# Performance work log

Hardware: AMD Instinct MI355X
Metric: run time of the kernel (lower is better)

Reference implementation:

```python
import jax, jax.numpy as jnp
import numpy as np

C_IN, C_HID, N_HEADS, N, B = 128, 32, 4, 384, 1
INF = 1e9


def setup_inputs() -> dict:
    key = jax.random.key(0)
    ks = jax.random.split(key, 8)
    s = 1.0 / np.sqrt(C_IN)
    return {
        "z": jax.random.normal(ks[0], (B, N, N, C_IN), dtype=jnp.float32),
        "mask": jnp.ones((B, N, N), dtype=jnp.float32),
        "ln_w": jnp.ones((C_IN,), dtype=jnp.float32),
        "ln_b": jnp.zeros((C_IN,), dtype=jnp.float32),
        "w_tri": jax.random.normal(ks[1], (C_IN, N_HEADS), dtype=jnp.float32) * s,
        "wq": jax.random.normal(ks[2], (C_IN, N_HEADS * C_HID), dtype=jnp.float32) * s,
        "wk": jax.random.normal(ks[3], (C_IN, N_HEADS * C_HID), dtype=jnp.float32) * s,
        "wv": jax.random.normal(ks[4], (C_IN, N_HEADS * C_HID), dtype=jnp.float32) * s,
        "wg": jax.random.normal(ks[5], (C_IN, N_HEADS * C_HID), dtype=jnp.float32) * s,
        "wo": jax.random.normal(ks[6], (N_HEADS * C_HID, C_IN), dtype=jnp.float32) * s,
    }


def _layer_norm(x, w, b, eps=1e-5):
    mu = jnp.mean(x, axis=-1, keepdims=True)
    var = jnp.var(x, axis=-1, keepdims=True)
    return (x - mu) * jax.lax.rsqrt(var + eps) * w + b


def reference(z, mask, ln_w, ln_b, w_tri, wq, wk, wv, wg, wo):
    # starting=True: attend over J (last pair axis); batch dims are (B, I)
    zn = _layer_norm(z, ln_w, ln_b)                       # [B,I,J,C]
    # biases
    mask_bias = (INF * (mask - 1.0))[:, :, None, None, :]  # [B,I,1,1,J]
    tri = jnp.einsum("bijc,ch->bhij", zn, w_tri)[:, None]  # [B,1,H,I,J]
    # projections -> [B,I,J,H,Ch]
    shp = zn.shape[:-1] + (N_HEADS, C_HID)
    q = (zn @ wq).reshape(shp) * (1.0 / np.sqrt(C_HID))
    k = (zn @ wk).reshape(shp)
    v = (zn @ wv).reshape(shp)
    scores = jnp.einsum("biqhc,bikhc->bihqk", q, k) + mask_bias + tri  # [B,I,H,J,J]
    a = jax.nn.softmax(scores, axis=-1)
    o = jnp.einsum("bihqk,bikhc->biqhc", a, v).reshape(zn.shape[:-1] + (N_HEADS * C_HID,))
    g = jax.nn.sigmoid(zn @ wg)                           # gated output (OpenFold-style)
    return (o * g) @ wo                                    # [B,I,J,C_in]
```

## Files before the change

### kernel.cpp

```cpp
#include <hip/hip_runtime.h>
#include <hip/hip_bf16.h>

#define NN 384
#define CIN 128
#define NH 4
#define CH 32
#define NPOS (NN * NN)
#define INFB 1e9f
#define QSCALE 0.17677669529663687f

typedef float f32x4 __attribute__((ext_vector_type(4)));
typedef short short8 __attribute__((ext_vector_type(8)));

__device__ __forceinline__ float bf2f(unsigned short u) {
    return __uint_as_float(((unsigned int)u) << 16);
}
__device__ __forceinline__ unsigned short f2bf(float f) {
    unsigned int u = __float_as_uint(f);
    u += 0x7fffu + ((u >> 16) & 1u);
    return (unsigned short)(u >> 16);
}
__device__ __forceinline__ unsigned int pack2bf(float a, float b) {
    return (unsigned int)f2bf(a) | ((unsigned int)f2bf(b) << 16);
}

__global__ __launch_bounds__(256) void ln_kernel(
    const float* __restrict__ z, const float* __restrict__ lnw, const float* __restrict__ lnb,
    const float* __restrict__ wtri,
    unsigned short* __restrict__ zn, unsigned short* __restrict__ trib)
{
    __shared__ float zt[32 * CIN];
    __shared__ float mu_s[32], rs_s[32];
    __shared__ float wt_s[CIN * NH];
    const int t = threadIdx.x;
    const long base = (long)blockIdx.x * (32 * CIN);

    #pragma unroll
    for (int r = 0; r < 16; ++r) zt[t + 256 * r] = z[base + t + 256 * r];
    wt_s[t] = wtri[t]; wt_s[t + 256] = wtri[t + 256];
    __syncthreads();

    {
        int p = t >> 3, s = t & 7;
        float sum = 0.f, sq = 0.f;
        for (int c = s; c < CIN; c += 8) { float x = zt[p * CIN + c]; sum += x; sq += x * x; }
        #pragma unroll
        for (int m = 1; m < 8; m <<= 1) { sum += __shfl_xor(sum, m); sq += __shfl_xor(sq, m); }
        if (s == 0) {
            float mu = sum * (1.f / CIN);
            float var = sq * (1.f / CIN) - mu * mu;
            mu_s[p] = mu; rs_s[p] = rsqrtf(var + 1e-5f);
        }
    }
    __syncthreads();
    #pragma unroll
    for (int r = 0; r < 16; ++r) {
        int idx = t + 256 * r; int p = idx >> 7, c = idx & 127;
        zt[idx] = (zt[idx] - mu_s[p]) * rs_s[p] * lnw[c] + lnb[c];
    }
    __syncthreads();

    unsigned int* zno = (unsigned int*)zn + (long)blockIdx.x * 2048;
    #pragma unroll
    for (int r = 0; r < 8; ++r) {
        int i32 = t + 256 * r;
        zno[i32] = pack2bf(zt[2 * i32], zt[2 * i32 + 1]);
    }

    if (t < 128) {
        int h = t >> 5, p = t & 31;
        float acc = 0.f;
        #pragma unroll 8
        for (int ii = 0; ii < CIN; ++ii) {
            int ci = (p + ii) & 127;
            acc = fmaf(zt[p * CIN + ci], wt_s[ci * NH + h], acc);
        }
        trib[(long)h * NPOS + (long)blockIdx.x * 32 + p] = f2bf(acc);
    }
}

__global__ __launch_bounds__(256) void wconv_kernel(
    const float* __restrict__ wq, const float* __restrict__ wk, const float* __restrict__ wv,
    const float* __restrict__ wg, const float* __restrict__ wo,
    unsigned short* __restrict__ wcat, unsigned short* __restrict__ wot)
{
    const int m = blockIdx.x, t = threadIdx.x;
    const float* W = (m == 0) ? wq : (m == 1) ? wk : (m == 2) ? wv : (m == 3) ? wg : wo;
    const float s = (m == 0) ? QSCALE : 1.0f;
    unsigned short* dst = (m < 4) ? (wcat + m * CIN * CIN) : wot;
    for (int idx = t; idx < CIN * CIN; idx += 256) {
        int n = idx >> 7, k = idx & 127;
        dst[idx] = f2bf(W[k * CIN + n] * s);
    }
}

__device__ __forceinline__ void gemm128_core(
    const unsigned short* __restrict__ Ag, const unsigned short* __restrict__ Bg,
    unsigned short* lsA, unsigned short* lsB, f32x4 acc[4][4], int t)
{
    const int lane = t & 63, w = t >> 6, l15 = lane & 15, hi = lane >> 4;
    #pragma unroll
    for (int it = 0; it < 8; ++it) {
        int row = w * 32 + it * 4 + hi;
        int cb = l15 * 16;
        uint4 va = *(const uint4*)((const char*)Ag + row * 256 + cb);
        uint4 vb = *(const uint4*)((const char*)Bg + row * 256 + cb);
        int sw = cb ^ ((row & 7) << 4);
        *(uint4*)((char*)lsA + row * 256 + sw) = va;
        *(uint4*)((char*)lsB + row * 256 + sw) = vb;
    }
    __syncthreads();
    const int wm = (w >> 1) * 64, wn = (w & 1) * 64;
    #pragma unroll
    for (int kk = 0; kk < 4; ++kk) {
        short8 a[4], b[4];
        #pragma unroll
        for (int f = 0; f < 4; ++f) {
            int ra = wm + f * 16 + l15;
            int rb = wn + f * 16 + l15;
            int c = kk * 64 + hi * 16;
            a[f] = *(const short8*)((const char*)lsA + ra * 256 + (c ^ ((ra & 7) << 4)));
            b[f] = *(const short8*)((const char*)lsB + rb * 256 + (c ^ ((rb & 7) << 4)));
        }
        #pragma unroll
        for (int mf = 0; mf < 4; ++mf)
            #pragma unroll
            for (int nf = 0; nf < 4; ++nf)
                acc[mf][nf] = __builtin_amdgcn_mfma_f32_16x16x32_bf16(a[mf], b[nf], acc[mf][nf], 0, 0, 0);
    }
}

__global__ __launch_bounds__(256) void proj_gemm_kernel(
    const unsigned short* __restrict__ zn, const unsigned short* __restrict__ wcat,
    unsigned short* __restrict__ qb, unsigned short* __restrict__ kb,
    unsigned short* __restrict__ vb, unsigned short* __restrict__ gb)
{
    __shared__ alignas(16) unsigned short lsA[128 * 128];
    __shared__ alignas(16) unsigned short lsB[128 * 128];
    const int t = threadIdx.x;
    const int mb = blockIdx.x, mat = blockIdx.y;
    f32x4 acc[4][4];
    #pragma unroll
    for (int i = 0; i < 4; ++i)
        #pragma unroll
        for (int j = 0; j < 4; ++j) acc[i][j] = (f32x4){0.f, 0.f, 0.f, 0.f};
    gemm128_core(zn + (long)mb * 128 * 128, wcat + mat * 128 * 128, lsA, lsB, acc, t);

    const int lane = t & 63, w = t >> 6, l15 = lane & 15, hi = lane >> 4;
    const int wm = (w >> 1) * 64, wn = (w & 1) * 64;
    unsigned short* dst = (mat == 0) ? qb : (mat == 1) ? kb : (mat == 2) ? vb : gb;
    #pragma unroll
    for (int mf = 0; mf < 4; ++mf)
        #pragma unroll
        for (int nf = 0; nf < 4; ++nf)
            #pragma unroll
            for (int r = 0; r < 4; ++r) {
                long pos = (long)mb * 128 + wm + mf * 16 + hi * 4 + r;
                int n = wn + nf * 16 + l15;
                float v = acc[mf][nf][r];
                if (mat == 3) v = 1.f / (1.f + __expf(-v));
                dst[pos * CIN + n] = f2bf(v);
            }
}

__global__ __launch_bounds__(256) void attn_kernel(
    const unsigned short* __restrict__ qb, const unsigned short* __restrict__ kb,
    const unsigned short* __restrict__ vb, const unsigned short* __restrict__ trib,
    const float* __restrict__ mask, unsigned short* __restrict__ ob)
{
    constexpr int KP = 40;
    constexpr int VP = 392;
    constexpr int PP = 392;
    __shared__ alignas(16) unsigned short Ks[NN * KP];
    __shared__ alignas(16) unsigned short VTs[CH * VP];
    __shared__ alignas(16) unsigned short Ps[4][16 * PP];
    __shared__ float biasS[NN];

    const int t = threadIdx.x;
    const int i = blockIdx.x >> 2, h = blockIdx.x & 3;
    const long rowbase = (long)i * NN;

    {
        const unsigned int* ksrc = (const unsigned int*)kb + rowbase * (CIN / 2) + h * (CH / 2);
        for (int idx = t; idx < NN * 16; idx += 256) {
            int row = idx >> 4, c2 = idx & 15;
            *(unsigned int*)&Ks[row * KP + c2 * 2] = ksrc[(long)row * 64 + c2];
        }
        for (int idx = t; idx < CH * NN; idx += 256) {
            int n = idx >> 5, c = idx & 31;
            VTs[c * VP + n] = vb[(rowbase + n) * CIN + h * CH + c];
        }
        for (int idx = t; idx < NN; idx += 256)
            biasS[idx] = INFB * (mask[rowbase + idx] - 1.f);
    }
    __syncthreads();

    const int lane = t & 63, w = t >> 6, l15 = lane & 15, hi = lane >> 4;
    unsigned short* Pw = Ps[w];
    const f32x4 zero4 = {0.f, 0.f, 0.f, 0.f};

    for (int mt = w; mt < NN / 16; mt += 4) {
        const int q0 = mt * 16;

        {
            const uint4* tsrc = (const uint4*)(trib + (long)h * NPOS + (long)q0 * NN);
            uint4* tdst = (uint4*)Pw;
            #pragma unroll
            for (int it = 0; it < 12; ++it)
                tdst[it * 64 + lane] = tsrc[it * 64 + lane];
        }

        const short8 aq = *(const short8*)(qb + (rowbase + q0 + l15) * CIN + h * CH + hi * 8);

        f32x4 acc[24];
        #pragma unroll
        for (int nf = 0; nf < 24; ++nf) {
            const short8 bk = *(const short8*)&Ks[(nf * 16 + l15) * KP + hi * 8];
            acc[nf] = __builtin_amdgcn_mfma_f32_16x16x32_bf16(aq, bk, zero4, 0, 0, 0);
        }

        float mx[4] = {-1e30f, -1e30f, -1e30f, -1e30f};
        #pragma unroll
        for (int nf = 0; nf < 24; ++nf)
            #pragma unroll
            for (int r = 0; r < 4; ++r) {
                float s = acc[nf][r] + biasS[nf * 16 + l15]
                        + bf2f(Pw[(4 * hi + r) * 384 + nf * 16 + l15]);
                acc[nf][r] = s;
                mx[r] = fmaxf(mx[r], s);
            }
        #pragma unroll
        for (int m2 = 1; m2 < 16; m2 <<= 1)
            #pragma unroll
            for (int r = 0; r < 4; ++r) mx[r] = fmaxf(mx[r], __shfl_xor(mx[r], m2));

        float sum[4] = {0.f, 0.f, 0.f, 0.f};
        #pragma unroll
        for (int nf = 0; nf < 24; ++nf)
            #pragma unroll
            for (int r = 0; r < 4; ++r) {
                float e = __expf(acc[nf][r] - mx[r]);
                acc[nf][r] = e; sum[r] += e;
            }
        #pragma unroll
        for (int m2 = 1; m2 < 16; m2 <<= 1)
            #pragma unroll
            for (int r = 0; r < 4; ++r) sum[r] += __shfl_xor(sum[r], m2);
        float inv[4];
        #pragma unroll
        for (int r = 0; r < 4; ++r) inv[r] = 1.f / sum[r];

        #pragma unroll
        for (int nf = 0; nf < 24; ++nf)
            #pragma unroll
            for (int r = 0; r < 4; ++r)
                Pw[(4 * hi + r) * PP + nf * 16 + l15] = f2bf(acc[nf][r]);

        f32x4 o0 = zero4, o1 = zero4;
        #pragma unroll
        for (int ks = 0; ks < 12; ++ks) {
            const short8 ap  = *(const short8*)&Pw[l15 * PP + ks * 32 + hi * 8];
            const short8 bv0 = *(const short8*)&VTs[l15 * VP + ks * 32 + hi * 8];
            const short8 bv1 = *(const short8*)&VTs[(16 + l15) * VP + ks * 32 + hi * 8];
            o0 = __builtin_amdgcn_mfma_f32_16x16x32_bf16(ap, bv0, o0, 0, 0, 0);
            o1 = __builtin_amdgcn_mfma_f32_16x16x32_bf16(ap, bv1, o1, 0, 0, 0);
        }

        #pragma unroll
        for (int r = 0; r < 4; ++r) {
            long qrow = rowbase + q0 + 4 * hi + r;
            ob[qrow * CIN + h * CH + l15]      = f2bf(o0[r] * inv[r]);
            ob[qrow * CIN + h * CH + 16 + l15] = f2bf(o1[r] * inv[r]);
        }
    }
}

__global__ __launch_bounds__(256) void og_kernel(
    const unsigned int* __restrict__ ob, const unsigned int* __restrict__ gb,
    unsigned int* __restrict__ og)
{
    const int n32 = NPOS * CIN / 2;
    for (long idx = (long)blockIdx.x * 256 + threadIdx.x; idx < n32; idx += (long)gridDim.x * 256) {
        unsigned int o = ob[idx], g = gb[idx];
        og[idx] = pack2bf(bf2f((unsigned short)o) * bf2f((unsigned short)g),
                          bf2f((unsigned short)(o >> 16)) * bf2f((unsigned short)(g >> 16)));
    }
}

__global__ __launch_bounds__(256) void out_gemm_kernel(
    const unsigned short* __restrict__ og, const unsigned short* __restrict__ wot,
    float* __restrict__ out)
{
    __shared__ alignas(16) unsigned short lsA[128 * 128];
    __shared__ alignas(16) unsigned short lsB[128 * 128];
    const int t = threadIdx.x;
    const int mb = blockIdx.x;
    f32x4 acc[4][4];
    #pragma unroll
    for (int i = 0; i < 4; ++i)
        #pragma unroll
        for (int j = 0; j < 4; ++j) acc[i][j] = (f32x4){0.f, 0.f, 0.f, 0.f};
    gemm128_core(og + (long)mb * 128 * 128, wot, lsA, lsB, acc, t);

    const int lane = t & 63, w = t >> 6, l15 = lane & 15, hi = lane >> 4;
    const int wm = (w >> 1) * 64, wn = (w & 1) * 64;
    #pragma unroll
    for (int mf = 0; mf < 4; ++mf)
        #pragma unroll
        for (int nf = 0; nf < 4; ++nf)
            #pragma unroll
            for (int r = 0; r < 4; ++r) {
                long pos = (long)mb * 128 + wm + mf * 16 + hi * 4 + r;
                int n = wn + nf * 16 + l15;
                out[pos * CIN + n] = acc[mf][nf][r];
            }
}

extern "C" void kernel_launch(void* const* d_in, const int* in_sizes, int n_in,
                              void* d_out, int out_size, void* d_ws, size_t ws_size,
                              hipStream_t stream)
{
    const float* z    = (const float*)d_in[0];
    const float* mask = (const float*)d_in[1];
    const float* lnw  = (const float*)d_in[2];
    const float* lnb  = (const float*)d_in[3];
    const float* wtri = (const float*)d_in[4];
    const float* wq   = (const float*)d_in[5];
    const float* wk   = (const float*)d_in[6];
    const float* wv   = (const float*)d_in[7];
    const float* wg   = (const float*)d_in[8];
    const float* wo   = (const float*)d_in[9];
    float* out = (float*)d_out;

    char* ws = (char*)d_ws;
    size_t off = 0;
    auto carve = [&](size_t bytes) -> void* {
        void* p = ws + off; off += (bytes + 255) & ~size_t(255); return p;
    };
    const size_t nelem = (size_t)NPOS * CIN;
    unsigned short* zn  = (unsigned short*)carve(nelem * 2);
    unsigned short* qb  = (unsigned short*)carve(nelem * 2);
    unsigned short* kb  = (unsigned short*)carve(nelem * 2);
    unsigned short* vb  = (unsigned short*)carve(nelem * 2);
    unsigned short* gb  = (unsigned short*)carve(nelem * 2);
    unsigned short* ob  = (unsigned short*)carve(nelem * 2);
    unsigned short* trib = (unsigned short*)carve((size_t)NH * NPOS * 2);
    unsigned short* wcat = (unsigned short*)carve((size_t)4 * CIN * CIN * 2);
    unsigned short* wot  = (unsigned short*)carve((size_t)CIN * CIN * 2);
    (void)ws_size; (void)in_sizes; (void)n_in; (void)out_size;

    hipLaunchKernelGGL(ln_kernel, dim3(NPOS / 32), dim3(256), 0, stream,
                       z, lnw, lnb, wtri, zn, trib);
    hipLaunchKernelGGL(wconv_kernel, dim3(5), dim3(256), 0, stream,
                       wq, wk, wv, wg, wo, wcat, wot);
    hipLaunchKernelGGL(proj_gemm_kernel, dim3(NPOS / 128, 4), dim3(256), 0, stream,
                       zn, wcat, qb, kb, vb, gb);
    hipLaunchKernelGGL(attn_kernel, dim3(NN * NH), dim3(256), 0, stream,
                       qb, kb, vb, trib, mask, ob);
    hipLaunchKernelGGL(og_kernel, dim3(2048), dim3(256), 0, stream,
                       (const unsigned int*)ob, (const unsigned int*)gb, (unsigned int*)zn);
    hipLaunchKernelGGL(out_gemm_kernel, dim3(NPOS / 128), dim3(256), 0, stream,
                       (const unsigned short*)zn, wot, out);
}
```

Baseline: 460.8 us.

## Restructure pipeline: fuse gating into attention, tri-bias into projection GEMM, exp2 softmax

```diff
diff --git a/kernel.cpp b/kernel.cpp
--- a/kernel.cpp
+++ b/kernel.cpp
@@ -7,10 +7,13 @@
 #define CH 32
 #define NPOS (NN * NN)
 #define INFB 1e9f
+#define LOG2E 1.4426950408889634f
 #define QSCALE 0.17677669529663687f
+#define QSB (QSCALE * LOG2E)
 
 typedef float f32x4 __attribute__((ext_vector_type(4)));
-typedef short short8 __attribute__((ext_vector_type(8)));
+typedef short bf16x8 __attribute__((ext_vector_type(8)));
+typedef short bf16x4 __attribute__((ext_vector_type(4)));
 
 __device__ __forceinline__ float bf2f(unsigned short u) {
     return __uint_as_float(((unsigned int)u) << 16);
@@ -26,291 +29,320 @@
 
 __global__ __launch_bounds__(256) void ln_kernel(
     const float* __restrict__ z, const float* __restrict__ lnw, const float* __restrict__ lnb,
-    const float* __restrict__ wtri,
-    unsigned short* __restrict__ zn, unsigned short* __restrict__ trib)
-{
-    __shared__ float zt[32 * CIN];
-    __shared__ float mu_s[32], rs_s[32];
-    __shared__ float wt_s[CIN * NH];
+    unsigned short* __restrict__ zn)
+{
     const int t = threadIdx.x;
-    const long base = (long)blockIdx.x * (32 * CIN);
-
-    #pragma unroll
-    for (int r = 0; r < 16; ++r) zt[t + 256 * r] = z[base + t + 256 * r];
-    wt_s[t] = wtri[t]; wt_s[t + 256] = wtri[t + 256];
-    __syncthreads();
-
-    {
-        int p = t >> 3, s = t & 7;
-        float sum = 0.f, sq = 0.f;
-        for (int c = s; c < CIN; c += 8) { float x = zt[p * CIN + c]; sum += x; sq += x * x; }
-        #pragma unroll
-        for (int m = 1; m < 8; m <<= 1) { sum += __shfl_xor(sum, m); sq += __shfl_xor(sq, m); }
-        if (s == 0) {
-            float mu = sum * (1.f / CIN);
-            float var = sq * (1.f / CIN) - mu * mu;
-            mu_s[p] = mu; rs_s[p] = rsqrtf(var + 1e-5f);
-        }
-    }
-    __syncthreads();
-    #pragma unroll
-    for (int r = 0; r < 16; ++r) {
-        int idx = t + 256 * r; int p = idx >> 7, c = idx & 127;
-        zt[idx] = (zt[idx] - mu_s[p]) * rs_s[p] * lnw[c] + lnb[c];
-    }
-    __syncthreads();
-
-    unsigned int* zno = (unsigned int*)zn + (long)blockIdx.x * 2048;
-    #pragma unroll
-    for (int r = 0; r < 8; ++r) {
-        int i32 = t + 256 * r;
-        zno[i32] = pack2bf(zt[2 * i32], zt[2 * i32 + 1]);
-    }
-
-    if (t < 128) {
-        int h = t >> 5, p = t & 31;
-        float acc = 0.f;
-        #pragma unroll 8
-        for (int ii = 0; ii < CIN; ++ii) {
-            int ci = (p + ii) & 127;
-            acc = fmaf(zt[p * CIN + ci], wt_s[ci * NH + h], acc);
-        }
-        trib[(long)h * NPOS + (long)blockIdx.x * 32 + p] = f2bf(acc);
-    }
+    const int l31 = t & 31;
+    const f32x4 lw = *(const f32x4*)(lnw + l31 * 4);
+    const f32x4 lb = *(const f32x4*)(lnb + l31 * 4);
+    #pragma unroll
+    for (int it = 0; it < 4; ++it) {
+        long row = (long)blockIdx.x * 32 + it * 8 + (threadIdx.x >> 5);
+        f32x4 v = *(const f32x4*)(z + row * CIN + l31 * 4);
+        float s = v[0] + v[1] + v[2] + v[3];
+        float q = v[0]*v[0] + v[1]*v[1] + v[2]*v[2] + v[3]*v[3];
+        #pragma unroll
+        for (int m2 = 1; m2 < 32; m2 <<= 1) { s += __shfl_xor(s, m2); q += __shfl_xor(q, m2); }
+        float mu = s * (1.f / CIN);
+        float rs = rsqrtf(q * (1.f / CIN) - mu * mu + 1e-5f);
+        uint2 o;
+        o.x = pack2bf((v[0]-mu)*rs*lw[0]+lb[0], (v[1]-mu)*rs*lw[1]+lb[1]);
+        o.y = pack2bf((v[2]-mu)*rs*lw[2]+lb[2], (v[3]-mu)*rs*lw[3]+lb[3]);
+        *(uint2*)(zn + row * CIN + l31 * 4) = o;
+    }
+    (void)t;
 }
 
 __global__ __launch_bounds__(256) void wconv_kernel(
     const float* __restrict__ wq, const float* __restrict__ wk, const float* __restrict__ wv,
-    const float* __restrict__ wg, const float* __restrict__ wo,
+    const float* __restrict__ wg, const float* __restrict__ wtri, const float* __restrict__ wo,
     unsigned short* __restrict__ wcat, unsigned short* __restrict__ wot)
 {
     const int m = blockIdx.x, t = threadIdx.x;
-    const float* W = (m == 0) ? wq : (m == 1) ? wk : (m == 2) ? wv : (m == 3) ? wg : wo;
-    const float s = (m == 0) ? QSCALE : 1.0f;
-    unsigned short* dst = (m < 4) ? (wcat + m * CIN * CIN) : wot;
     for (int idx = t; idx < CIN * CIN; idx += 256) {
         int n = idx >> 7, k = idx & 127;
-        dst[idx] = f2bf(W[k * CIN + n] * s);
-    }
-}
-
-__device__ __forceinline__ void gemm128_core(
-    const unsigned short* __restrict__ Ag, const unsigned short* __restrict__ Bg,
-    unsigned short* lsA, unsigned short* lsB, f32x4 acc[4][4], int t)
-{
-    const int lane = t & 63, w = t >> 6, l15 = lane & 15, hi = lane >> 4;
-    #pragma unroll
-    for (int it = 0; it < 8; ++it) {
-        int row = w * 32 + it * 4 + hi;
-        int cb = l15 * 16;
-        uint4 va = *(const uint4*)((const char*)Ag + row * 256 + cb);
-        uint4 vb = *(const uint4*)((const char*)Bg + row * 256 + cb);
-        int sw = cb ^ ((row & 7) << 4);
-        *(uint4*)((char*)lsA + row * 256 + sw) = va;
-        *(uint4*)((char*)lsB + row * 256 + sw) = vb;
-    }
-    __syncthreads();
-    const int wm = (w >> 1) * 64, wn = (w & 1) * 64;
-    #pragma unroll
-    for (int kk = 0; kk < 4; ++kk) {
-        short8 a[4], b[4];
-        #pragma unroll
-        for (int f = 0; f < 4; ++f) {
-            int ra = wm + f * 16 + l15;
-            int rb = wn + f * 16 + l15;
-            int c = kk * 64 + hi * 16;
-            a[f] = *(const short8*)((const char*)lsA + ra * 256 + (c ^ ((ra & 7) << 4)));
-            b[f] = *(const short8*)((const char*)lsB + rb * 256 + (c ^ ((rb & 7) << 4)));
-        }
-        #pragma unroll
-        for (int mf = 0; mf < 4; ++mf)
-            #pragma unroll
-            for (int nf = 0; nf < 4; ++nf)
-                acc[mf][nf] = __builtin_amdgcn_mfma_f32_16x16x32_bf16(a[mf], b[nf], acc[mf][nf], 0, 0, 0);
-    }
-}
-
-__global__ __launch_bounds__(256) void proj_gemm_kernel(
+        if (m < 4) {
+            const float* W = (m == 0) ? wq : (m == 1) ? wk : (m == 2) ? wv : wg;
+            float s = (m == 0) ? QSB : 1.0f;
+            wcat[m * CIN * CIN + idx] = f2bf(W[k * CIN + n] * s);
+        } else if (m == 4) {
+            wcat[4 * CIN * CIN + idx] = (n < NH) ? f2bf(wtri[k * NH + n] * LOG2E) : (unsigned short)0;
+        } else {
+            wot[idx] = f2bf(wo[k * CIN + n]);
+        }
+    }
+}
+
+__global__ __launch_bounds__(256, 2) void proj_kernel(
     const unsigned short* __restrict__ zn, const unsigned short* __restrict__ wcat,
     unsigned short* __restrict__ qb, unsigned short* __restrict__ kb,
-    unsigned short* __restrict__ vb, unsigned short* __restrict__ gb)
-{
-    __shared__ alignas(16) unsigned short lsA[128 * 128];
-    __shared__ alignas(16) unsigned short lsB[128 * 128];
-    const int t = threadIdx.x;
-    const int mb = blockIdx.x, mat = blockIdx.y;
-    f32x4 acc[4][4];
-    #pragma unroll
-    for (int i = 0; i < 4; ++i)
-        #pragma unroll
-        for (int j = 0; j < 4; ++j) acc[i][j] = (f32x4){0.f, 0.f, 0.f, 0.f};
-    gemm128_core(zn + (long)mb * 128 * 128, wcat + mat * 128 * 128, lsA, lsB, acc, t);
-
-    const int lane = t & 63, w = t >> 6, l15 = lane & 15, hi = lane >> 4;
-    const int wm = (w >> 1) * 64, wn = (w & 1) * 64;
-    unsigned short* dst = (mat == 0) ? qb : (mat == 1) ? kb : (mat == 2) ? vb : gb;
-    #pragma unroll
-    for (int mf = 0; mf < 4; ++mf)
-        #pragma unroll
-        for (int nf = 0; nf < 4; ++nf)
-            #pragma unroll
-            for (int r = 0; r < 4; ++r) {
-                long pos = (long)mb * 128 + wm + mf * 16 + hi * 4 + r;
-                int n = wn + nf * 16 + l15;
-                float v = acc[mf][nf][r];
-                if (mat == 3) v = 1.f / (1.f + __expf(-v));
-                dst[pos * CIN + n] = f2bf(v);
-            }
-}
-
-__global__ __launch_bounds__(256) void attn_kernel(
-    const unsigned short* __restrict__ qb, const unsigned short* __restrict__ kb,
-    const unsigned short* __restrict__ vb, const unsigned short* __restrict__ trib,
-    const float* __restrict__ mask, unsigned short* __restrict__ ob)
-{
-    constexpr int KP = 40;
-    constexpr int VP = 392;
-    constexpr int PP = 392;
-    __shared__ alignas(16) unsigned short Ks[NN * KP];
-    __shared__ alignas(16) unsigned short VTs[CH * VP];
-    __shared__ alignas(16) unsigned short Ps[4][16 * PP];
-    __shared__ float biasS[NN];
-
-    const int t = threadIdx.x;
-    const int i = blockIdx.x >> 2, h = blockIdx.x & 3;
-    const long rowbase = (long)i * NN;
-
-    {
-        const unsigned int* ksrc = (const unsigned int*)kb + rowbase * (CIN / 2) + h * (CH / 2);
-        for (int idx = t; idx < NN * 16; idx += 256) {
-            int row = idx >> 4, c2 = idx & 15;
-            *(unsigned int*)&Ks[row * KP + c2 * 2] = ksrc[(long)row * 64 + c2];
-        }
-        for (int idx = t; idx < CH * NN; idx += 256) {
-            int n = idx >> 5, c = idx & 31;
-            VTs[c * VP + n] = vb[(rowbase + n) * CIN + h * CH + c];
-        }
-        for (int idx = t; idx < NN; idx += 256)
-            biasS[idx] = INFB * (mask[rowbase + idx] - 1.f);
-    }
-    __syncthreads();
-
-    const int lane = t & 63, w = t >> 6, l15 = lane & 15, hi = lane >> 4;
-    unsigned short* Pw = Ps[w];
-    const f32x4 zero4 = {0.f, 0.f, 0.f, 0.f};
-
-    for (int mt = w; mt < NN / 16; mt += 4) {
-        const int q0 = mt * 16;
-
-        {
-            const uint4* tsrc = (const uint4*)(trib + (long)h * NPOS + (long)q0 * NN);
-            uint4* tdst = (uint4*)Pw;
-            #pragma unroll
-            for (int it = 0; it < 12; ++it)
-                tdst[it * 64 + lane] = tsrc[it * 64 + lane];
-        }
-
-        const short8 aq = *(const short8*)(qb + (rowbase + q0 + l15) * CIN + h * CH + hi * 8);
-
-        f32x4 acc[24];
-        #pragma unroll
-        for (int nf = 0; nf < 24; ++nf) {
-            const short8 bk = *(const short8*)&Ks[(nf * 16 + l15) * KP + hi * 8];
-            acc[nf] = __builtin_amdgcn_mfma_f32_16x16x32_bf16(aq, bk, zero4, 0, 0, 0);
-        }
-
-        float mx[4] = {-1e30f, -1e30f, -1e30f, -1e30f};
-        #pragma unroll
-        for (int nf = 0; nf < 24; ++nf)
-            #pragma unroll
-            for (int r = 0; r < 4; ++r) {
-                float s = acc[nf][r] + biasS[nf * 16 + l15]
-                        + bf2f(Pw[(4 * hi + r) * 384 + nf * 16 + l15]);
-                acc[nf][r] = s;
-                mx[r] = fmaxf(mx[r], s);
-            }
-        #pragma unroll
-        for (int m2 = 1; m2 < 16; m2 <<= 1)
-            #pragma unroll
-            for (int r = 0; r < 4; ++r) mx[r] = fmaxf(mx[r], __shfl_xor(mx[r], m2));
-
-        float sum[4] = {0.f, 0.f, 0.f, 0.f};
-        #pragma unroll
-        for (int nf = 0; nf < 24; ++nf)
-            #pragma unroll
-            for (int r = 0; r < 4; ++r) {
-                float e = __expf(acc[nf][r] - mx[r]);
-                acc[nf][r] = e; sum[r] += e;
-            }
-        #pragma unroll
-        for (int m2 = 1; m2 < 16; m2 <<= 1)
-            #pragma unroll
-            for (int r = 0; r < 4; ++r) sum[r] += __shfl_xor(sum[r], m2);
-        float inv[4];
-        #pragma unroll
-        for (int r = 0; r < 4; ++r) inv[r] = 1.f / sum[r];
-
-        #pragma unroll
-        for (int nf = 0; nf < 24; ++nf)
-            #pragma unroll
-            for (int r = 0; r < 4; ++r)
-                Pw[(4 * hi + r) * PP + nf * 16 + l15] = f2bf(acc[nf][r]);
-
-        f32x4 o0 = zero4, o1 = zero4;
-        #pragma unroll
-        for (int ks = 0; ks < 12; ++ks) {
-            const short8 ap  = *(const short8*)&Pw[l15 * PP + ks * 32 + hi * 8];
-            const short8 bv0 = *(const short8*)&VTs[l15 * VP + ks * 32 + hi * 8];
-            const short8 bv1 = *(const short8*)&VTs[(16 + l15) * VP + ks * 32 + hi * 8];
-            o0 = __builtin_amdgcn_mfma_f32_16x16x32_bf16(ap, bv0, o0, 0, 0, 0);
-            o1 = __builtin_amdgcn_mfma_f32_16x16x32_bf16(ap, bv1, o1, 0, 0, 0);
-        }
-
-        #pragma unroll
-        for (int r = 0; r < 4; ++r) {
-            long qrow = rowbase + q0 + 4 * hi + r;
-            ob[qrow * CIN + h * CH + l15]      = f2bf(o0[r] * inv[r]);
-            ob[qrow * CIN + h * CH + 16 + l15] = f2bf(o1[r] * inv[r]);
-        }
-    }
-}
-
-__global__ __launch_bounds__(256) void og_kernel(
-    const unsigned int* __restrict__ ob, const unsigned int* __restrict__ gb,
-    unsigned int* __restrict__ og)
-{
-    const int n32 = NPOS * CIN / 2;
-    for (long idx = (long)blockIdx.x * 256 + threadIdx.x; idx < n32; idx += (long)gridDim.x * 256) {
-        unsigned int o = ob[idx], g = gb[idx];
-        og[idx] = pack2bf(bf2f((unsigned short)o) * bf2f((unsigned short)g),
-                          bf2f((unsigned short)(o >> 16)) * bf2f((unsigned short)(g >> 16)));
-    }
-}
-
-__global__ __launch_bounds__(256) void out_gemm_kernel(
-    const unsigned short* __restrict__ og, const unsigned short* __restrict__ wot,
-    float* __restrict__ out)
+    unsigned short* __restrict__ vb, unsigned short* __restrict__ gb,
+    unsigned short* __restrict__ trib)
 {
     __shared__ alignas(16) unsigned short lsA[128 * 128];
     __shared__ alignas(16) unsigned short lsB[128 * 128];
     const int t = threadIdx.x;
     const int mb = blockIdx.x;
+    const int lane = t & 63, w = t >> 6, l15 = lane & 15, hig = lane >> 4;
+
+    {
+        const unsigned short* Ag = zn + (long)mb * 16384;
+        #pragma unroll
+        for (int it = 0; it < 8; ++it) {
+            int row = w * 32 + it * 4 + hig; int cb = l15 * 16;
+            uint4 v = *(const uint4*)((const char*)Ag + row * 256 + cb);
+            *(uint4*)((char*)lsA + row * 256 + (cb ^ ((row & 7) << 4))) = v;
+        }
+    }
+    auto stageB = [&](int mat) {
+        const unsigned short* Bg = wcat + mat * 16384;
+        #pragma unroll
+        for (int it = 0; it < 8; ++it) {
+            int row = w * 32 + it * 4 + hig; int cb = l15 * 16;
+            uint4 v = *(const uint4*)((const char*)Bg + row * 256 + cb);
+            *(uint4*)((char*)lsB + row * 256 + (cb ^ ((row & 7) << 4))) = v;
+        }
+    };
+    stageB(0);
+    __syncthreads();
+
+    const int wm = (w >> 1) * 64, wn = (w & 1) * 64;
+    bf16x8 a[4][4];
+    #pragma unroll
+    for (int kk = 0; kk < 4; ++kk)
+        #pragma unroll
+        for (int mf = 0; mf < 4; ++mf) {
+            int ra = wm + mf * 16 + l15;
+            a[kk][mf] = *(const bf16x8*)((const char*)lsA + ra * 256 + ((kk * 64 + hig * 16) ^ ((ra & 7) << 4)));
+        }
+
+    for (int mat = 0;;) {
+        f32x4 acc[4][4];
+        #pragma unroll
+        for (int i = 0; i < 4; ++i)
+            #pragma unroll
+            for (int j = 0; j < 4; ++j) acc[i][j] = (f32x4){0.f, 0.f, 0.f, 0.f};
+        #pragma unroll
+        for (int kk = 0; kk < 4; ++kk) {
+            bf16x8 b[4];
+            #pragma unroll
+            for (int nf = 0; nf < 4; ++nf) {
+                int rb = wn + nf * 16 + l15;
+                b[nf] = *(const bf16x8*)((const char*)lsB + rb * 256 + ((kk * 64 + hig * 16) ^ ((rb & 7) << 4)));
+            }
+            #pragma unroll
+            for (int mf = 0; mf < 4; ++mf)
+                #pragma unroll
+                for (int nf = 0; nf < 4; ++nf)
+                    acc[mf][nf] = __builtin_amdgcn_mfma_f32_16x16x32_bf16(a[kk][mf], b[nf], acc[mf][nf], 0, 0, 0);
+        }
+        __syncthreads();
+        if (mat < 4) stageB(mat + 1);
+
+        if (mat < 4) {
+            unsigned short* dst = (mat == 0) ? qb : (mat == 1) ? kb : (mat == 2) ? vb : gb;
+            #pragma unroll
+            for (int mf = 0; mf < 4; ++mf)
+                #pragma unroll
+                for (int nf = 0; nf < 4; ++nf)
+                    #pragma unroll
+                    for (int r = 0; r < 4; ++r) {
+                        long pos = (long)mb * 128 + wm + mf * 16 + hig * 4 + r;
+                        int n = wn + nf * 16 + l15;
+                        float v = acc[mf][nf][r];
+                        if (mat == 3) v = 1.f / (1.f + __expf(-v));
+                        dst[pos * CIN + n] = f2bf(v);
+                    }
+        } else {
+            if (wn == 0 && l15 < NH) {
+                #pragma unroll
+                for (int mf = 0; mf < 4; ++mf)
+                    #pragma unroll
+                    for (int r = 0; r < 4; ++r) {
+                        long pos = (long)mb * 128 + wm + mf * 16 + hig * 4 + r;
+                        trib[(long)l15 * NPOS + pos] = f2bf(acc[mf][0][r]);
+                    }
+            }
+        }
+        if (mat == 4) break;
+        ++mat;
+        __syncthreads();
+    }
+}
+
+__global__ __launch_bounds__(256, 2) void attn_kernel(
+    const unsigned short* __restrict__ qb, const unsigned short* __restrict__ kb,
+    const unsigned short* __restrict__ vb, const unsigned short* __restrict__ gb,
+    const unsigned short* __restrict__ trib, const float* __restrict__ mask,
+    unsigned short* __restrict__ ogb)
+{
+    constexpr int KP = 40;
+    constexpr int VP = 392;
+    __shared__ alignas(16) unsigned short Ks[NN * KP];
+    __shared__ alignas(16) unsigned short VTs[CH * VP];
+    __shared__ alignas(16) unsigned short Ps[4][2][16 * 64];
+    __shared__ float biasS[NN];
+
+    const int t = threadIdx.x;
+    const int bid = blockIdx.x;
+    const int wg = (bid & 7) * 192 + (bid >> 3);
+    const int i = wg >> 2, h = wg & 3;
+    const long rowbase = (long)i * NN;
+
+    {
+        const unsigned int* ksrc = (const unsigned int*)kb + rowbase * 64 + h * 16;
+        for (int idx = t; idx < NN * 16; idx += 256) {
+            int row = idx >> 4, c2 = idx & 15;
+            *(unsigned int*)&Ks[row * KP + c2 * 2] = ksrc[(long)row * 64 + c2];
+        }
+        for (int idx = t; idx < CH * NN; idx += 256) {
+            int n = idx >> 5, c = idx & 31;
+            VTs[c * VP + n] = vb[(rowbase + n) * CIN + h * CH + c];
+        }
+        for (int idx = t; idx < NN; idx += 256)
+            biasS[idx] = (INFB * LOG2E) * (mask[rowbase + idx] - 1.f);
+    }
+    __syncthreads();
+
+    const int lane = t & 63, w = t >> 6, l15 = lane & 15, hig = lane >> 4;
+
+    bf16x8 bv[12][2];
+    #pragma unroll
+    for (int ks = 0; ks < 12; ++ks)
+        #pragma unroll
+        for (int hf = 0; hf < 2; ++hf) {
+            int c = hf * 16 + l15;
+            bv[ks][hf] = *(const bf16x8*)&VTs[c * VP + ks * 32 + hig * 8];
+        }
+
+    char* Pw = (char*)Ps[w];
+
+    for (int mt = w; mt < NN / 16; mt += 4) {
+        const int q0 = mt * 16;
+        const bf16x8 aq = *(const bf16x8*)(qb + (rowbase + q0 + l15) * CIN + h * CH + hig * 8);
+        const unsigned short* trow = trib + (long)h * NPOS + (long)(q0 + l15) * NN + hig * 4;
+
+        f32x4 acc[24];
+        #pragma unroll
+        for (int nf = 0; nf < 24; ++nf) {
+            bf16x4 t4 = *(const bf16x4*)(trow + nf * 16);
+            f32x4 ci;
+            #pragma unroll
+            for (int r = 0; r < 4; ++r)
+                ci[r] = bf2f((unsigned short)t4[r]) + biasS[nf * 16 + hig * 4 + r];
+            const int krow = nf * 16 + l15;
+            const bf16x8 ak = *(const bf16x8*)&Ks[krow * KP + hig * 8];
+            acc[nf] = __builtin_amdgcn_mfma_f32_16x16x32_bf16(ak, aq, ci, 0, 0, 0);
+        }
+
+        float mx = -3e38f;
+        #pragma unroll
+        for (int nf = 0; nf < 24; ++nf)
+            #pragma unroll
+            for (int r = 0; r < 4; ++r) mx = fmaxf(mx, acc[nf][r]);
+        mx = fmaxf(mx, __shfl_xor(mx, 16));
+        mx = fmaxf(mx, __shfl_xor(mx, 32));
+        float sum = 0.f;
+        #pragma unroll
+        for (int nf = 0; nf < 24; ++nf)
+            #pragma unroll
+            for (int r = 0; r < 4; ++r) {
+                float p = exp2f(acc[nf][r] - mx);
+                acc[nf][r] = p; sum += p;
+            }
+        sum += __shfl_xor(sum, 16);
+        sum += __shfl_xor(sum, 32);
+        const float inv = 1.0f / sum;
+
+        f32x4 o0 = {0.f,0.f,0.f,0.f}, o1 = {0.f,0.f,0.f,0.f};
+        __builtin_amdgcn_s_setprio(1);
+        #pragma unroll
+        for (int ch = 0; ch < 6; ++ch) {
+            char* Pb = Pw + (ch & 1) * 2048;
+            #pragma unroll
+            for (int nfl = 0; nfl < 4; ++nfl) {
+                int nf = ch * 4 + nfl;
+                uint2 wv;
+                wv.x = pack2bf(acc[nf][0], acc[nf][1]);
+                wv.y = pack2bf(acc[nf][2], acc[nf][3]);
+                *(uint2*)(Pb + l15 * 128 + ((nfl * 32 + hig * 8) ^ ((l15 & 7) << 4))) = wv;
+            }
+            #pragma unroll
+            for (int ksl = 0; ksl < 2; ++ksl) {
+                int ks = ch * 2 + ksl;
+                bf16x8 ap = *(const bf16x8*)(Pb + l15 * 128 + ((ksl * 64 + hig * 16) ^ ((l15 & 7) << 4)));
+                o0 = __builtin_amdgcn_mfma_f32_16x16x32_bf16(ap, bv[ks][0], o0, 0, 0, 0);
+                o1 = __builtin_amdgcn_mfma_f32_16x16x32_bf16(ap, bv[ks][1], o1, 0, 0, 0);
+            }
+        }
+        __builtin_amdgcn_s_setprio(0);
+
+        #pragma unroll
+        for (int r = 0; r < 4; ++r) {
+            float iv = __shfl(inv, hig * 4 + r);
+            long qrow = rowbase + q0 + hig * 4 + r;
+            float g0 = bf2f(gb[qrow * CIN + h * CH + l15]);
+            float g1 = bf2f(gb[qrow * CIN + h * CH + 16 + l15]);
+            ogb[qrow * CIN + h * CH + l15]      = f2bf(o0[r] * iv * g0);
+            ogb[qrow * CIN + h * CH + 16 + l15] = f2bf(o1[r] * iv * g1);
+        }
+    }
+}
+
+__global__ __launch_bounds__(256, 2) void out_gemm_kernel(
+    const unsigned short* __restrict__ og, const unsigned short* __restrict__ wot,
+    float* __restrict__ out)
+{
+    __shared__ alignas(16) unsigned short lsA[128 * 128];
+    __shared__ alignas(16) unsigned short lsB[128 * 128];
+    const int t = threadIdx.x;
+    const int mb = blockIdx.x;
+    const int lane = t & 63, w = t >> 6, l15 = lane & 15, hig = lane >> 4;
+
+    {
+        const unsigned short* Ag = og + (long)mb * 16384;
+        #pragma unroll
+        for (int it = 0; it < 8; ++it) {
+            int row = w * 32 + it * 4 + hig; int cb = l15 * 16;
+            uint4 va = *(const uint4*)((const char*)Ag + row * 256 + cb);
+            uint4 vb4 = *(const uint4*)((const char*)wot + row * 256 + cb);
+            int sw = cb ^ ((row & 7) << 4);
+            *(uint4*)((char*)lsA + row * 256 + sw) = va;
+            *(uint4*)((char*)lsB + row * 256 + sw) = vb4;
+        }
+    }
+    __syncthreads();
+
+    const int wm = (w >> 1) * 64, wn = (w & 1) * 64;
     f32x4 acc[4][4];
     #pragma unroll
     for (int i = 0; i < 4; ++i)
         #pragma unroll
         for (int j = 0; j < 4; ++j) acc[i][j] = (f32x4){0.f, 0.f, 0.f, 0.f};
-    gemm128_core(og + (long)mb * 128 * 128, wot, lsA, lsB, acc, t);
-
-    const int lane = t & 63, w = t >> 6, l15 = lane & 15, hi = lane >> 4;
-    const int wm = (w >> 1) * 64, wn = (w & 1) * 64;
+    #pragma unroll
+    for (int kk = 0; kk < 4; ++kk) {
+        bf16x8 a[4], b[4];
+        #pragma unroll
+        for (int f = 0; f < 4; ++f) {
+            int ra = wm + f * 16 + l15;
+            int rb = wn + f * 16 + l15;
+            int c = kk * 64 + hig * 16;
+            a[f] = *(const bf16x8*)((const char*)lsA + ra * 256 + (c ^ ((ra & 7) << 4)));
+            b[f] = *(const bf16x8*)((const char*)lsB + rb * 256 + (c ^ ((rb & 7) << 4)));
+        }
+        #pragma unroll
+        for (int mf = 0; mf < 4; ++mf)
+            #pragma unroll
+            for (int nf = 0; nf < 4; ++nf)
+                acc[mf][nf] = __builtin_amdgcn_mfma_f32_16x16x32_bf16(a[mf], b[nf], acc[mf][nf], 0, 0, 0);
+    }
     #pragma unroll
     for (int mf = 0; mf < 4; ++mf)
         #pragma unroll
         for (int nf = 0; nf < 4; ++nf)
             #pragma unroll
             for (int r = 0; r < 4; ++r) {
-                long pos = (long)mb * 128 + wm + mf * 16 + hi * 4 + r;
+                long pos = (long)mb * 128 + wm + mf * 16 + hig * 4 + r;
                 int n = wn + nf * 16 + l15;
                 out[pos * CIN + n] = acc[mf][nf][r];
             }
@@ -338,27 +370,25 @@
         void* p = ws + off; off += (bytes + 255) & ~size_t(255); return p;
     };
     const size_t nelem = (size_t)NPOS * CIN;
-    unsigned short* zn  = (unsigned short*)carve(nelem * 2);
-    unsigned short* qb  = (unsigned short*)carve(nelem * 2);
-    unsigned short* kb  = (unsigned short*)carve(nelem * 2);
-    unsigned short* vb  = (unsigned short*)carve(nelem * 2);
-    unsigned short* gb  = (unsigned short*)carve(nelem * 2);
-    unsigned short* ob  = (unsigned short*)carve(nelem * 2);
+    unsigned short* zn   = (unsigned short*)carve(nelem * 2);
+    unsigned short* qb   = (unsigned short*)carve(nelem * 2);
+    unsigned short* kb   = (unsigned short*)carve(nelem * 2);
+    unsigned short* vb   = (unsigned short*)carve(nelem * 2);
+    unsigned short* gb   = (unsigned short*)carve(nelem * 2);
+    unsigned short* ogb  = (unsigned short*)carve(nelem * 2);
     unsigned short* trib = (unsigned short*)carve((size_t)NH * NPOS * 2);
-    unsigned short* wcat = (unsigned short*)carve((size_t)4 * CIN * CIN * 2);
+    unsigned short* wcat = (unsigned short*)carve((size_t)5 * CIN * CIN * 2);
     unsigned short* wot  = (unsigned short*)carve((size_t)CIN * CIN * 2);
     (void)ws_size; (void)in_sizes; (void)n_in; (void)out_size;
 
     hipLaunchKernelGGL(ln_kernel, dim3(NPOS / 32), dim3(256), 0, stream,
-                       z, lnw, lnb, wtri, zn, trib);
-    hipLaunchKernelGGL(wconv_kernel, dim3(5), dim3(256), 0, stream,
-                       wq, wk, wv, wg, wo, wcat, wot);
-    hipLaunchKernelGGL(proj_gemm_kernel, dim3(NPOS / 128, 4), dim3(256), 0, stream,
-                       zn, wcat, qb, kb, vb, gb);
+                       z, lnw, lnb, zn);
+    hipLaunchKernelGGL(wconv_kernel, dim3(6), dim3(256), 0, stream,
+                       wq, wk, wv, wg, wtri, wo, wcat, wot);
+    hipLaunchKernelGGL(proj_kernel, dim3(NPOS / 128), dim3(256), 0, stream,
+                       zn, wcat, qb, kb, vb, gb, trib);
     hipLaunchKernelGGL(attn_kernel, dim3(NN * NH), dim3(256), 0, stream,
-                       qb, kb, vb, trib, mask, ob);
-    hipLaunchKernelGGL(og_kernel, dim3(2048), dim3(256), 0, stream,
-                       (const unsigned int*)ob, (const unsigned int*)gb, (unsigned int*)zn);
+                       qb, kb, vb, gb, trib, mask, ogb);
     hipLaunchKernelGGL(out_gemm_kernel, dim3(NPOS / 128), dim3(256), 0, stream,
-                       (const unsigned short*)zn, wot, out);
-}
+                       ogb, wot, out);
+}
```

Result: slower. 749.7 us (+62.7%).
